# Performance work log

Measured on AMD Instinct MI355X. Metric: run time of the kernel, lower is better.

Reference implementation:

```python
import jax, jax.numpy as jnp
import numpy as np
from jax import lax

DIM = 256
HEADS = 8
DIM_HEAD = 64
INNER = HEADS * DIM_HEAD  # 512
K = 3
PAD = K // 2
KV_STRIDE = 2
SCALE = DIM_HEAD ** -0.5
BN_EPS = 1e-5


def _dw_block(x, w_dw, g, b, m, v, w_pw, stride):
    """depthwise conv -> batchnorm (eval) -> 1x1 conv. x: [B,C,H,W]."""
    c = x.shape[1]
    h = lax.conv_general_dilated(
        x, w_dw, window_strides=(stride, stride),
        padding=[(PAD, PAD), (PAD, PAD)],
        feature_group_count=c,
        dimension_numbers=('NCHW', 'OIHW', 'NCHW'))
    inv = lax.rsqrt(v + BN_EPS)
    h = (h - m[None, :, None, None]) * (g * inv)[None, :, None, None] + b[None, :, None, None]
    return jnp.einsum('oc,bchw->bohw', w_pw, h)


def _heads_flat(t):
    # [B, h*d, H, W] -> [B, h, d, H*W]
    B, hd, H, W = t.shape
    return t.reshape(B, HEADS, DIM_HEAD, H * W)


def _cross_attn(q, k, v, Hq, Wq):
    # q: [B,h,d,i], k/v: [B,h,d,j]
    dots = jnp.einsum('bhdi,bhdj->bhij', q, k) * SCALE
    attn = jax.nn.softmax(dots, axis=-1)
    out = jnp.einsum('bhij,bhdj->bhdi', attn, v)
    B = q.shape[0]
    return out.reshape(B, INNER, Hq, Wq)


def _forward(x, y, q_dw_w, q_bn_gamma, q_bn_beta, q_bn_mean, q_bn_var, q_pw_w,
             kv_dw_w, kv_bn_gamma, kv_bn_beta, kv_bn_mean, kv_bn_var, kv_pw_w,
             out_w, out_b):
    B, _, Hx, Wx = x.shape
    _, _, Hy, Wy = y.shape

    qx = _heads_flat(_dw_block(x, q_dw_w, q_bn_gamma, q_bn_beta, q_bn_mean, q_bn_var, q_pw_w, 1))
    kvx = _dw_block(x, kv_dw_w, kv_bn_gamma, kv_bn_beta, kv_bn_mean, kv_bn_var, kv_pw_w, KV_STRIDE)
    kx, vx = map(_heads_flat, jnp.split(kvx, 2, axis=1))

    qy = _heads_flat(_dw_block(y, q_dw_w, q_bn_gamma, q_bn_beta, q_bn_mean, q_bn_var, q_pw_w, 1))
    kvy = _dw_block(y, kv_dw_w, kv_bn_gamma, kv_bn_beta, kv_bn_mean, kv_bn_var, kv_pw_w, KV_STRIDE)
    ky, vy = map(_heads_flat, jnp.split(kvy, 2, axis=1))

    outx = _cross_attn(qx, ky, vy, Hx, Wx)   # x queries attend to y keys/values
    outy = _cross_attn(qy, kx, vx, Hy, Wy)   # y queries attend to x keys/values

    def proj(o):
        return jnp.einsum('oc,bchw->bohw', out_w, o) + out_b[None, :, None, None]

    return proj(outx), proj(outy)


def setup_inputs() -> dict:
    key = jax.random.key(0)
    ks = jax.random.split(key, 8)
    B, H, W = 8, 32, 32
    return {
        'x': jax.random.normal(ks[0], (B, DIM, H, W), jnp.float32),
        'y': jax.random.normal(ks[1], (B, DIM, H, W), jnp.float32),
        'q_dw_w': jax.random.normal(ks[2], (DIM, 1, K, K), jnp.float32) * 0.1,
        'q_bn_gamma': jnp.ones((DIM,), jnp.float32),
        'q_bn_beta': jnp.zeros((DIM,), jnp.float32),
        'q_bn_mean': jnp.zeros((DIM,), jnp.float32),
        'q_bn_var': jnp.ones((DIM,), jnp.float32),
        'q_pw_w': jax.random.normal(ks[3], (INNER, DIM), jnp.float32) * (DIM ** -0.5),
        'kv_dw_w': jax.random.normal(ks[4], (DIM, 1, K, K), jnp.float32) * 0.1,
        'kv_bn_gamma': jnp.ones((DIM,), jnp.float32),
        'kv_bn_beta': jnp.zeros((DIM,), jnp.float32),
        'kv_bn_mean': jnp.zeros((DIM,), jnp.float32),
        'kv_bn_var': jnp.ones((DIM,), jnp.float32),
        'kv_pw_w': jax.random.normal(ks[5], (2 * INNER, DIM), jnp.float32) * (DIM ** -0.5),
        'out_w': jax.random.normal(ks[6], (DIM, INNER), jnp.float32) * (INNER ** -0.5),
        'out_b': jnp.zeros((DIM,), jnp.float32),
    }


def reference(x, y, q_dw_w, q_bn_gamma, q_bn_beta, q_bn_mean, q_bn_var, q_pw_w,
              kv_dw_w, kv_bn_gamma, kv_bn_beta, kv_bn_mean, kv_bn_var, kv_pw_w,
              out_w, out_b):
    return _forward(x, y, q_dw_w, q_bn_gamma, q_bn_beta, q_bn_mean, q_bn_var, q_pw_w,
                    kv_dw_w, kv_bn_gamma, kv_bn_beta, kv_bn_mean, kv_bn_var, kv_pw_w,
                    out_w, out_b)
```

## Files before the change

### kernel.cpp

```cpp
#include <hip/hip_runtime.h>

#define BN_EPS 1e-5f
#define ATT_SCALE 0.125f

typedef _Float16 half_t;
typedef _Float16 half8 __attribute__((ext_vector_type(8)));
typedef _Float16 half4 __attribute__((ext_vector_type(4)));
typedef float f32x4 __attribute__((ext_vector_type(4)));

__device__ __forceinline__ void gll16(const void* g, void* l) {
    __builtin_amdgcn_global_load_lds((const __attribute__((address_space(1))) void*)g,
                                     (__attribute__((address_space(3))) void*)l, 16, 0, 0);
}

template<int N>
__device__ __forceinline__ void vmwait() {
    asm volatile("s_waitcnt vmcnt(%0)" :: "i"(N) : "memory");
}

__device__ void prep_body8(
    int base, int c,
    const float* qg, const float* qb, const float* qm, const float* qv, const float* qpw,
    const float* kg, const float* kbt, const float* km, const float* kvv, const float* kvpw,
    const float* outw,
    half_t* wq, half_t* wkv, half_t* wout, float* bq, float* bkv, float* red)
{
    #pragma unroll
    for (int oo = 0; oo < 8; ++oo) {
        int o = base + oo;
        if (o >= 1536) {
            int ro = o - 1536;
            #pragma unroll
            for (int ci = 0; ci < 2; ++ci) {
                int cc = ci * 256 + c;
                float wv = outw[(size_t)ro * 512 + cc];
                half_t hh = (half_t)wv;
                wout[(size_t)ro * 1024 + cc]       = hh;
                wout[(size_t)ro * 1024 + 512 + cc] = (half_t)(wv - (float)hh);
            }
            continue;
        }
        const float *g, *b, *m, *v, *w; half_t* we; float* be;
        if (o < 512) {
            g = qg; b = qb; m = qm; v = qv;
            w = qpw + (size_t)o * 256; we = wq + (size_t)o * 512; be = bq + o;
        } else {
            int ro = o - 512;
            g = kg; b = kbt; m = km; v = kvv;
            w = kvpw + (size_t)ro * 256; we = wkv + (size_t)ro * 512; be = bkv + ro;
        }
        float s  = g[c] * rsqrtf(v[c] + BN_EPS);
        float tt = b[c] - m[c] * s;
        float wv = w[c];
        float wsv = wv * s;
        half_t hh = (half_t)wsv;
        we[c]       = hh;
        we[256 + c] = (half_t)(wsv - (float)hh);
        float partial = wv * tt;
        #pragma unroll
        for (int off = 32; off > 0; off >>= 1)
            partial += __shfl_down(partial, off, 64);
        if ((c & 63) == 0) red[c >> 6] = partial;
        __syncthreads();
        if (c == 0) *be = red[0] + red[1] + red[2] + red[3];
        __syncthreads();
    }
}

__device__ void dw_body(
    int rp, int img, int cc, float* sin,
    const float* x, const float* y,
    const float* qdw, const float* kvdw,
    half_t* qB, half_t* kvB)
{
    const float* in = (img < 8) ? x + (size_t)img * 256 * 1024
                                : y + (size_t)(img - 8) * 256 * 1024;
    int t = threadIdx.x;
    int ch = t & 63, cg = t >> 6;
    int r0 = 2 * rp - 1;
    #pragma unroll
    for (int u = t; u < 1024; u += 256) {
        int c = u >> 4, row = (u >> 2) & 3, pi = u & 3;
        sin[c * 148 + row * 36 + (pi < 2 ? pi : 32 + pi)] = 0.f;
    }
    #pragma unroll
    for (int ii = 0; ii < 8; ++ii) {
        int u = ii * 256 + t;
        int sch = u >> 5, row = (u >> 3) & 3, seg = u & 7;
        int gr = r0 + row;
        float4 v4 = {0.f, 0.f, 0.f, 0.f};
        if (gr >= 0 && gr < 32)
            v4 = *(const float4*)(in + (size_t)(cc * 64 + sch) * 1024 + gr * 32 + seg * 4);
        float* d = &sin[sch * 148 + row * 36 + 2 + seg * 4];
        d[0] = v4.x; d[1] = v4.y; d[2] = v4.z; d[3] = v4.w;
    }
    __syncthreads();
    int gch = cc * 64 + ch;
    float wq9[9], wk9[9];
    #pragma unroll
    for (int i = 0; i < 9; ++i) { wq9[i] = qdw[gch * 9 + i]; wk9[i] = kvdw[gch * 9 + i]; }
    float rowv[4][12];
    const float* base = &sin[ch * 148];
    #pragma unroll
    for (int rr = 0; rr < 4; ++rr) {
        *(float4*)&rowv[rr][0] = *(const float4*)(base + rr * 36 + cg * 8);
        *(float4*)&rowv[rr][4] = *(const float4*)(base + rr * 36 + cg * 8 + 4);
        *(float4*)&rowv[rr][8] = *(const float4*)(base + rr * 36 + cg * 8 + 8);
    }
    #pragma unroll
    for (int r = 0; r < 2; ++r) {
        #pragma unroll
        for (int c8 = 0; c8 < 8; ++c8) {
            float acc = 0.f;
            #pragma unroll
            for (int dr = 0; dr < 3; ++dr)
                #pragma unroll
                for (int dc = 0; dc < 3; ++dc)
                    acc += wq9[dr * 3 + dc] * rowv[r + dr][c8 + dc + 1];
            half_t hh = (half_t)acc;
            size_t p = (size_t)img * 1024 + (2 * rp + r) * 32 + cg * 8 + c8;
            qB[p * 512 + gch]       = hh;
            qB[p * 512 + 256 + gch] = (half_t)(acc - (float)hh);
        }
    }
    #pragma unroll
    for (int c4 = 0; c4 < 4; ++c4) {
        float acc = 0.f;
        #pragma unroll
        for (int dr = 0; dr < 3; ++dr)
            #pragma unroll
            for (int dc = 0; dc < 3; ++dc)
                acc += wk9[dr * 3 + dc] * rowv[dr][2 * c4 + dc + 1];
        half_t hh = (half_t)acc;
        size_t p = (size_t)img * 256 + rp * 16 + cg * 4 + c4;
        kvB[p * 512 + gch]       = hh;
        kvB[p * 512 + 256 + gch] = (half_t)(acc - (float)hh);
    }
}

__global__ __launch_bounds__(256) void prep_dw_kernel(
    const float* __restrict__ x, const float* __restrict__ y,
    const float* __restrict__ qdw, const float* __restrict__ kvdw,
    const float* __restrict__ qg, const float* __restrict__ qb,
    const float* __restrict__ qm, const float* __restrict__ qv,
    const float* __restrict__ qpw,
    const float* __restrict__ kg, const float* __restrict__ kbt,
    const float* __restrict__ km, const float* __restrict__ kvv,
    const float* __restrict__ kvpw,
    const float* __restrict__ outw,
    half_t* __restrict__ wq, half_t* __restrict__ wkv, half_t* __restrict__ wout,
    float* __restrict__ bq, float* __restrict__ bkv,
    half_t* __restrict__ qB, half_t* __restrict__ kvB)
{
    __shared__ __align__(16) float smem[64 * 148];
    int bx = blockIdx.x;
    if (bx < 1024)
        dw_body((bx >> 4) & 15, bx & 15, bx >> 8, smem, x, y, qdw, kvdw, qB, kvB);
    else
        prep_body8((bx - 1024) * 8, threadIdx.x, qg, qb, qm, qv, qpw,
                   kg, kbt, km, kvv, kvpw, outw, wq, wkv, wout, bq, bkv, smem);
}

template<int MT, int NT, int WGM, int WGN, int NTHR, int MODE, int KTOT>
__device__ __forceinline__ void gemm_worker(
    char* lds, const half_t* Ab, const half_t* Bb,
    void* outBuf, const float* bias,
    int NPX, int img, int m0, int n0, float scale)
{
    constexpr int TM = WGM * MT * 16, TN = WGN * NT * 16;
    constexpr int BUF = (TM + TN) * 128;
    constexpr int NC = KTOT / 32;
    constexpr int GCNT = 8 * (TM + TN) / NTHR;
    int t = threadIdx.x, w = t >> 6, lane = t & 63, quad = lane >> 4, l15 = lane & 15;
    int wm = w % WGM, wn = w / WGM;
    f32x4 acc[MT][NT] = {};

    auto stage = [&](int kh, int p) {
        char* Ah = lds + p * BUF;
        char* Al = Ah + TM * 64;
        char* Bh = Ah + TM * 128;
        char* Bl = Bh + TN * 64;
        #pragma unroll
        for (int ii = 0; ii < TM * 4 / NTHR; ++ii) {
            int u = ii * NTHR + t;
            int mt = u >> 6, q = (u >> 4) & 3, r = u & 15;
            const half_t* g = Ab + (size_t)(mt * 16 + r) * (2 * KTOT) + kh + q * 8;
            gll16(g,        Ah + (u & ~63) * 16);
            gll16(g + KTOT, Al + (u & ~63) * 16);
        }
        #pragma unroll
        for (int ii = 0; ii < TN * 4 / NTHR; ++ii) {
            int u = ii * NTHR + t;
            int nt = u >> 6, q = (u >> 4) & 3, r = u & 15;
            const half_t* g = Bb + (size_t)(nt * 16 + r) * (2 * KTOT) + kh + q * 8;
            gll16(g,        Bh + (u & ~63) * 16);
            gll16(g + KTOT, Bl + (u & ~63) * 16);
        }
    };

    stage(0, 0);
    for (int kc = 0; kc < NC; ++kc) {
        if (kc + 1 < NC) { stage((kc + 1) * 32, (kc + 1) & 1); vmwait<GCNT>(); }
        else             { vmwait<0>(); }
        __builtin_amdgcn_s_barrier();
        __builtin_amdgcn_sched_barrier(0);
        char* Ah = lds + (kc & 1) * BUF;
        char* Al = Ah + TM * 64;
        char* Bh = Ah + TM * 128;
        char* Bl = Bh + TN * 64;
        half8 afh[MT], afl[MT];
        #pragma unroll
        for (int mi = 0; mi < MT; ++mi) {
            afh[mi] = *(half8*)(Ah + (wm * MT + mi) * 1024 + lane * 16);
            afl[mi] = *(half8*)(Al + (wm * MT + mi) * 1024 + lane * 16);
        }
        __builtin_amdgcn_s_setprio(1);
        #pragma unroll
        for (int ni = 0; ni < NT; ++ni) {
            half8 bh = *(half8*)(Bh + (wn * NT + ni) * 1024 + lane * 16);
            half8 bl = *(half8*)(Bl + (wn * NT + ni) * 1024 + lane * 16);
            #pragma unroll
            for (int mi = 0; mi < MT; ++mi) {
                acc[mi][ni] = __builtin_amdgcn_mfma_f32_16x16x32_f16(afh[mi], bh, acc[mi][ni], 0, 0, 0);
                acc[mi][ni] = __builtin_amdgcn_mfma_f32_16x16x32_f16(afh[mi], bl, acc[mi][ni], 0, 0, 0);
                acc[mi][ni] = __builtin_amdgcn_mfma_f32_16x16x32_f16(afl[mi], bh, acc[mi][ni], 0, 0, 0);
            }
        }
        __builtin_amdgcn_s_setprio(0);
        __builtin_amdgcn_s_barrier();
        __builtin_amdgcn_sched_barrier(0);
    }

    if (MODE == 2) {
        #pragma unroll
        for (int mi = 0; mi < MT; ++mi) {
            int mrow0 = m0 + wm * MT * 16 + mi * 16 + quad * 4;
            #pragma unroll
            for (int ni = 0; ni < NT; ++ni) {
                int col = n0 + wn * NT * 16 + ni * 16 + l15;
                f32x4 a = acc[mi][ni];
                float* op = (float*)outBuf + (size_t)img * 256 * NPX;
                #pragma unroll
                for (int r = 0; r < 4; ++r)
                    op[(size_t)(mrow0 + r) * NPX + col] = a[r] + bias[mrow0 + r];
            }
        }
    } else {
        __syncthreads();
        float* tbuf = (float*)lds;
        constexpr int TP = 40;
        #pragma unroll
        for (int qtr = 0; qtr < TM / 32; ++qtr) {
            #pragma unroll
            for (int mi = 0; mi < MT; ++mi) {
                int rowblk = wm * MT * 16 + mi * 16;
                if (rowblk >= qtr * 32 && rowblk < qtr * 32 + 32) {
                    int mloc = rowblk - qtr * 32 + quad * 4;
                    #pragma unroll
                    for (int ni = 0; ni < NT; ++ni) {
                        int nloc = wn * NT * 16 + ni * 16 + l15;
                        #pragma unroll
                        for (int r = 0; r < 4; ++r) {
                            float vv = acc[mi][ni][r];
                            if (MODE == 0) vv = (vv + bias[m0 + rowblk + quad * 4 + r]) * scale;
                            else           vv = vv + bias[n0 + nloc];
                            tbuf[nloc * TP + mloc + r] = vv;
                        }
                    }
                }
            }
            __syncthreads();
            #pragma unroll
            for (int it = 0; it < (TN * 4) / NTHR; ++it) {
                int u = it * NTHR + t;
                int n = u >> 2, mg = u & 3;
                float vv[8];
                *(float4*)&vv[0] = *(const float4*)&tbuf[n * TP + mg * 8];
                *(float4*)&vv[4] = *(const float4*)&tbuf[n * TP + mg * 8 + 4];
                half8 hv, lv;
                #pragma unroll
                for (int j = 0; j < 8; ++j) {
                    half_t hh = (half_t)vv[j];
                    hv[j] = hh; lv[j] = (half_t)(vv[j] - (float)hh);
                }
                int mglob = m0 + qtr * 32 + mg * 8;
                if (MODE == 0) {
                    int h = mglob >> 6, d0 = mglob & 63;
                    half_t* op = (half_t*)outBuf + ((size_t)(img * 8 + h) * NPX + n0 + n) * 128 + d0;
                    *(half8*)op = hv;
                    *(half8*)(op + 64) = lv;
                } else {
                    int nn = n0 + n, h = nn >> 6, d = nn & 63;
                    int j0 = mglob;
                    half_t* op = (half_t*)outBuf + (size_t)(img * 8 + h) * 32768
                               + (j0 >> 5) * 4096 + ((d >> 4) & 3) * 512 + ((j0 >> 4) & 1) * 256
                               + ((j0 >> 2) & 3) * 64 + (d & 15) * 4;
                    half4 a0 = {hv[0], hv[1], hv[2], hv[3]};
                    half4 a1 = {hv[4], hv[5], hv[6], hv[7]};
                    half4 b0 = {lv[0], lv[1], lv[2], lv[3]};
                    half4 b1 = {lv[4], lv[5], lv[6], lv[7]};
                    *(half4*)op               = a0;
                    *(half4*)(op + 64)        = a1;
                    *(half4*)(op + 2048)      = b0;
                    *(half4*)(op + 2048 + 64) = b1;
                }
            }
            __syncthreads();
        }
    }
}

__global__ __launch_bounds__(512, 4) void qkv_kernel(
    const half_t* __restrict__ wq, const half_t* __restrict__ wkv,
    const half_t* __restrict__ qB, const half_t* __restrict__ kvB,
    const float* __restrict__ bq, const float* __restrict__ bkv,
    half_t* __restrict__ qpr, half_t* __restrict__ kpr, half_t* __restrict__ vpr)
{
    __shared__ __align__(16) char lds[65536];
    int tile = blockIdx.x, img = blockIdx.z;
    if (tile < 32) {
        int m0 = (tile >> 3) * 128, n0 = (tile & 7) * 128;
        gemm_worker<2, 4, 4, 2, 512, 0, 256>(lds,
            wq + (size_t)m0 * 512,
            qB + (size_t)img * (1024 * 512) + (size_t)n0 * 512,
            qpr, bq, 1024, img, m0, n0, ATT_SCALE);
    } else if (tile < 40) {
        int tt = tile - 32;
        int m0 = (tt >> 1) * 128, n0 = (tt & 1) * 128;
        gemm_worker<2, 4, 4, 2, 512, 0, 256>(lds,
            wkv + (size_t)m0 * 512,
            kvB + (size_t)img * (256 * 512) + (size_t)n0 * 512,
            kpr, bkv, 256, img, m0, n0, 1.0f);
    } else {
        int tt = tile - 40;
        int m0 = (tt >> 2) * 128, n0 = (tt & 3) * 128;
        gemm_worker<2, 4, 4, 2, 512, 1, 256>(lds,
            kvB + (size_t)img * (256 * 512) + (size_t)m0 * 512,
            wkv + (size_t)(512 + n0) * 512,
            vpr, bkv + 512, 512, img, m0, n0, 1.0f);
    }
}

__global__ __launch_bounds__(512, 4) void out_kernel(
    const half_t* __restrict__ wout, const half_t* __restrict__ attp,
    const float* __restrict__ outb, float* __restrict__ out)
{
    __shared__ __align__(16) char lds[65536];
    int tile = blockIdx.x, img = blockIdx.z;
    int m0 = (tile >> 3) * 128, n0 = (tile & 7) * 128;
    gemm_worker<2, 4, 4, 2, 512, 2, 512>(lds,
        wout + (size_t)m0 * 1024,
        attp + (size_t)img * (1024 * 1024) + (size_t)n0 * 1024,
        out, outb, 1024, img, m0, n0, 1.0f);
}

__global__ __launch_bounds__(512, 4) void attn_fused(
    const half_t* __restrict__ qb, const half_t* __restrict__ kb,
    const half_t* __restrict__ vb, half_t* __restrict__ att)
{
    __shared__ __align__(16) char lds[33792];
    int ic = blockIdx.y;
    int img = blockIdx.x & 15, h = blockIdx.x >> 4;
    int partner = img ^ 8;
    int t = threadIdx.x, w = t >> 6, lane = t & 63, quad = lane >> 4, l15 = lane & 15;
    const half_t* qp = qb + ((size_t)(img * 8 + h) * 1024 + ic * 128) * 128;
    const half_t* kp = kb + (size_t)(partner * 8 + h) * 256 * 128;
    const half_t* vp = vb + (size_t)(partner * 8 + h) * 32768;

    half8 qh[2], ql[2];
    #pragma unroll
    for (int kcs = 0; kcs < 2; ++kcs) {
        const half_t* qr = qp + (size_t)(w * 16 + l15) * 128 + kcs * 32 + quad * 8;
        qh[kcs] = *(const half8*)qr;
        ql[kcs] = *(const half8*)(qr + 64);
    }

    auto stageC = [&](int c) {
        char* buf = lds + (c & 3) * 8192;
        if (c < 8) {
            int sb = t >> 6, li = t & 63;
            int plane = sb >> 2, ntr = (sb >> 1) & 1, kcs = sb & 1;
            const half_t* g = kp + (size_t)(c * 32 + ntr * 16 + (li & 15)) * 128
                                 + plane * 64 + kcs * 32 + (li >> 4) * 8;
            gll16(g, buf + (t & ~63) * 16);
        } else {
            gll16(vp + (size_t)(c - 8) * 4096 + t * 8, buf + (t & ~63) * 16);
        }
    };

    f32x4 sacc[16] = {};
    f32x4 oacc[4] = {};
    float mx = 0.f, lsum = 0.f;

    stageC(0); stageC(1); stageC(2);

    #pragma unroll
    for (int c = 0; c < 16; ++c) {
        if (c < 14)       vmwait<2>();
        else if (c == 14) vmwait<1>();
        else              vmwait<0>();
        __builtin_amdgcn_s_barrier();
        __builtin_amdgcn_sched_barrier(0);
        if (c + 3 < 16) stageC(c + 3);
        const char* buf = lds + (c & 3) * 8192;
        if (c < 8) {
            __builtin_amdgcn_s_setprio(1);
            #pragma unroll
            for (int kcs = 0; kcs < 2; ++kcs)
                #pragma unroll
                for (int ntr = 0; ntr < 2; ++ntr) {
                    half8 kh = *(const half8*)(buf + (ntr * 2 + kcs) * 1024 + lane * 16);
                    half8 kl = *(const half8*)(buf + 4096 + (ntr * 2 + kcs) * 1024 + lane * 16);
                    f32x4 s = sacc[c * 2 + ntr];
                    s = __builtin_amdgcn_mfma_f32_16x16x32_f16(kh, qh[kcs], s, 0, 0, 0);
                    s = __builtin_amdgcn_mfma_f32_16x16x32_f16(kh, ql[kcs], s, 0, 0, 0);
                    s = __builtin_amdgcn_mfma_f32_16x16x32_f16(kl, qh[kcs], s, 0, 0, 0);
                    sacc[c * 2 + ntr] = s;
                }
            __builtin_amdgcn_s_setprio(0);
        } else {
            if (c == 8) {
                float m_ = sacc[0][0];
                #pragma unroll
                for (int ti = 0; ti < 16; ++ti)
                    #pragma unroll
                    for (int r = 0; r < 4; ++r) m_ = fmaxf(m_, sacc[ti][r]);
                m_ = fmaxf(m_, __shfl_xor(m_, 16, 64));
                mx = fmaxf(m_, __shfl_xor(m_, 32, 64));
            }
            int jc = c - 8;
            half4 pb[2][2];
            #pragma unroll
            for (int kk = 0; kk < 2; ++kk) {
                f32x4 s = sacc[jc * 2 + kk];
                #pragma unroll
                for (int e = 0; e < 4; ++e) {
                    float pv = __expf(s[e] - mx);
                    lsum += pv;
                    half_t hh = (half_t)pv;
                    pb[kk][0][e] = hh;
                    pb[kk][1][e] = (half_t)(pv - (float)hh);
                }
            }
            __builtin_amdgcn_s_setprio(1);
            #pragma unroll
            for (int mt = 0; mt < 4; ++mt) {
                #pragma unroll
                for (int kk = 0; kk < 2; ++kk) {
                    half4 vh = *(const half4*)(buf + (mt * 2 + kk) * 512 + lane * 8);
                    half4 vl = *(const half4*)(buf + 4096 + (mt * 2 + kk) * 512 + lane * 8);
                    f32x4 o = oacc[mt];
                    o = __builtin_amdgcn_mfma_f32_16x16x16f16(vh, pb[kk][0], o, 0, 0, 0);
                    o = __builtin_amdgcn_mfma_f32_16x16x16f16(vh, pb[kk][1], o, 0, 0, 0);
                    o = __builtin_amdgcn_mfma_f32_16x16x16f16(vl, pb[kk][0], o, 0, 0, 0);
                    oacc[mt] = o;
                }
            }
            __builtin_amdgcn_s_setprio(0);
        }
    }

    lsum += __shfl_xor(lsum, 16, 64);
    lsum += __shfl_xor(lsum, 32, 64);
    float inv = 1.f / lsum;

    __syncthreads();
    #pragma unroll
    for (int mt = 0; mt < 4; ++mt)
        #pragma unroll
        for (int r = 0; r < 4; ++r) {
            float vv = oacc[mt][r] * inv;
            half_t hh = (half_t)vv;
            int row = w * 16 + l15;
            int d = mt * 16 + quad * 4 + r;
            *(half_t*)(lds + (row * 132 + d) * 2)      = hh;
            *(half_t*)(lds + (row * 132 + 64 + d) * 2) = (half_t)(vv - (float)hh);
        }
    __syncthreads();
    #pragma unroll
    for (int ii = 0; ii < 4; ++ii) {
        int u = ii * 512 + t;
        int i = u >> 4, seg = (u >> 3) & 1, p8 = u & 7;
        half8 val = *(const half8*)(lds + (i * 132 + seg * 64 + p8 * 8) * 2);
        *(half8*)(att + ((size_t)img * 1024 + ic * 128 + i) * 1024
                  + seg * 512 + h * 64 + p8 * 8) = val;
    }
}

extern "C" void kernel_launch(void* const* d_in, const int* in_sizes, int n_in,
                              void* d_out, int out_size, void* d_ws, size_t ws_size,
                              hipStream_t stream) {
    const float* x    = (const float*)d_in[0];
    const float* y    = (const float*)d_in[1];
    const float* qdw  = (const float*)d_in[2];
    const float* qg   = (const float*)d_in[3];
    const float* qbb  = (const float*)d_in[4];
    const float* qm   = (const float*)d_in[5];
    const float* qv   = (const float*)d_in[6];
    const float* qpw  = (const float*)d_in[7];
    const float* kvdw = (const float*)d_in[8];
    const float* kg   = (const float*)d_in[9];
    const float* kb_  = (const float*)d_in[10];
    const float* km   = (const float*)d_in[11];
    const float* kvv  = (const float*)d_in[12];
    const float* kvpw = (const float*)d_in[13];
    const float* outw = (const float*)d_in[14];
    const float* outb = (const float*)d_in[15];

    char* ws = (char*)d_ws;
    half_t* wq   = (half_t*)(ws);
    half_t* wkv  = (half_t*)(ws + 524288);
    half_t* wout = (half_t*)(ws + 1572864);
    float*  bq   = (float*) (ws + 2097152);
    float*  bkv  = (float*) (ws + 2099200);
    half_t* qpr  = (half_t*)(ws + 2103296);
    half_t* kpr  = (half_t*)(ws + 35657728);
    half_t* vpr  = (half_t*)(ws + 44046336);
    half_t* qB   = (half_t*)(ws + 52434944);
    half_t* kvB  = (half_t*)(ws + 69212160);
    half_t* attp = (half_t*)(ws + 52434944);

    prep_dw_kernel<<<1248, 256, 0, stream>>>(
        x, y, qdw, kvdw, qg, qbb, qm, qv, qpw, kg, kb_, km, kvv, kvpw, outw,
        wq, wkv, wout, bq, bkv, qB, kvB);

    qkv_kernel<<<dim3(48, 1, 16), 512, 0, stream>>>(
        wq, wkv, qB, kvB, bq, bkv, qpr, kpr, vpr);

    attn_fused<<<dim3(128, 8, 1), 512, 0, stream>>>(qpr, kpr, vpr, attp);

    out_kernel<<<dim3(16, 1, 16), 512, 0, stream>>>(wout, attp, outb, (float*)d_out);
}
```

Measured before the change: 197.7 us.

## Replace out-projection GEMM with dedicated 128x64 tile kernel and doubled grid

The output projection no longer goes through the generic gemm_worker. It now has its own kernel with 128x64 tiles, a double-buffered LDS pipeline filled by direct global-to-LDS loads, and 2x2 MFMA tiles per warp, launched on twice as many blocks. The MODE 2 epilogue in gemm_worker is removed because nothing uses it anymore. The aim is more blocks to spread across CUs and better latency hiding, at the cost of less data reuse per tile and more reloading of the weight tiles.

```diff
diff --git a/kernel.cpp b/kernel.cpp
--- a/kernel.cpp
+++ b/kernel.cpp
@@ -231,82 +231,66 @@
         __builtin_amdgcn_sched_barrier(0);
     }
 
-    if (MODE == 2) {
+    __syncthreads();
+    float* tbuf = (float*)lds;
+    constexpr int TP = 40;
+    #pragma unroll
+    for (int qtr = 0; qtr < TM / 32; ++qtr) {
         #pragma unroll
         for (int mi = 0; mi < MT; ++mi) {
-            int mrow0 = m0 + wm * MT * 16 + mi * 16 + quad * 4;
-            #pragma unroll
-            for (int ni = 0; ni < NT; ++ni) {
-                int col = n0 + wn * NT * 16 + ni * 16 + l15;
-                f32x4 a = acc[mi][ni];
-                float* op = (float*)outBuf + (size_t)img * 256 * NPX;
+            int rowblk = wm * MT * 16 + mi * 16;
+            if (rowblk >= qtr * 32 && rowblk < qtr * 32 + 32) {
+                int mloc = rowblk - qtr * 32 + quad * 4;
                 #pragma unroll
-                for (int r = 0; r < 4; ++r)
-                    op[(size_t)(mrow0 + r) * NPX + col] = a[r] + bias[mrow0 + r];
-            }
-        }
-    } else {
-        __syncthreads();
-        float* tbuf = (float*)lds;
-        constexpr int TP = 40;
-        #pragma unroll
-        for (int qtr = 0; qtr < TM / 32; ++qtr) {
-            #pragma unroll
-            for (int mi = 0; mi < MT; ++mi) {
-                int rowblk = wm * MT * 16 + mi * 16;
-                if (rowblk >= qtr * 32 && rowblk < qtr * 32 + 32) {
-                    int mloc = rowblk - qtr * 32 + quad * 4;
+                for (int ni = 0; ni < NT; ++ni) {
+                    int nloc = wn * NT * 16 + ni * 16 + l15;
                     #pragma unroll
-                    for (int ni = 0; ni < NT; ++ni) {
-                        int nloc = wn * NT * 16 + ni * 16 + l15;
-                        #pragma unroll
-                        for (int r = 0; r < 4; ++r) {
-                            float vv = acc[mi][ni][r];
-                            if (MODE == 0) vv = (vv + bias[m0 + rowblk + quad * 4 + r]) * scale;
-                            else           vv = vv + bias[n0 + nloc];
-                            tbuf[nloc * TP + mloc + r] = vv;
-                        }
+                    for (int r = 0; r < 4; ++r) {
+                        float vv = acc[mi][ni][r];
+                        if (MODE == 0) vv = (vv + bias[m0 + rowblk + quad * 4 + r]) * scale;
+                        else           vv = vv + bias[n0 + nloc];
+                        tbuf[nloc * TP + mloc + r] = vv;
                     }
                 }
             }
-            __syncthreads();
-            #pragma unroll
-            for (int it = 0; it < (TN * 4) / NTHR; ++it) {
-                int u = it * NTHR + t;
-                int n = u >> 2, mg = u & 3;
-                float vv[8];
-                *(float4*)&vv[0] = *(const float4*)&tbuf[n * TP + mg * 8];
-                *(float4*)&vv[4] = *(const float4*)&tbuf[n * TP + mg * 8 + 4];
-                half8 hv, lv;
-                #pragma unroll
-                for (int j = 0; j < 8; ++j) {
-                    half_t hh = (half_t)vv[j];
-                    hv[j] = hh; lv[j] = (half_t)(vv[j] - (float)hh);
-                }
-                int mglob = m0 + qtr * 32 + mg * 8;
-                if (MODE == 0) {
-                    int h = mglob >> 6, d0 = mglob & 63;
-                    half_t* op = (half_t*)outBuf + ((size_t)(img * 8 + h) * NPX + n0 + n) * 128 + d0;
-                    *(half8*)op = hv;
-                    *(half8*)(op + 64) = lv;
-                } else {
-                    int nn = n0 + n, h = nn >> 6, d = nn & 63;
-                    int j0 = mglob;
-                    half_t* op = (half_t*)outBuf + (size_t)(img * 8 + h) * 32768
-                               + (j0 >> 5) * 4096 + ((d >> 4) & 3) * 512 + ((j0 >> 4) & 1) * 256
-                               + ((j0 >> 2) & 3) * 64 + (d & 15) * 4;
-                    half4 a0 = {hv[0], hv[1], hv[2], hv[3]};
-                    half4 a1 = {hv[4], hv[5], hv[6], hv[7]};
-                    half4 b0 = {lv[0], lv[1], lv[2], lv[3]};
-                    half4 b1 = {lv[4], lv[5], lv[6], lv[7]};
-                    *(half4*)op               = a0;
-                    *(half4*)(op + 64)        = a1;
-                    *(half4*)(op + 2048)      = b0;
-                    *(half4*)(op + 2048 + 64) = b1;
-                }
-            }
-            __syncthreads();
-        }
+        }
+        __syncthreads();
+        #pragma unroll
+        for (int it = 0; it < (TN * 4) / NTHR; ++it) {
+            int u = it * NTHR + t;
+            int n = u >> 2, mg = u & 3;
+            float vv[8];
+            *(float4*)&vv[0] = *(const float4*)&tbuf[n * TP + mg * 8];
+            *(float4*)&vv[4] = *(const float4*)&tbuf[n * TP + mg * 8 + 4];
+            half8 hv, lv;
+            #pragma unroll
+            for (int j = 0; j < 8; ++j) {
+                half_t hh = (half_t)vv[j];
+                hv[j] = hh; lv[j] = (half_t)(vv[j] - (float)hh);
+            }
+            int mglob = m0 + qtr * 32 + mg * 8;
+            if (MODE == 0) {
+                int h = mglob >> 6, d0 = mglob & 63;
+                half_t* op = (half_t*)outBuf + ((size_t)(img * 8 + h) * NPX + n0 + n) * 128 + d0;
+                *(half8*)op = hv;
+                *(half8*)(op + 64) = lv;
+            } else {
+                int nn = n0 + n, h = nn >> 6, d = nn & 63;
+                int j0 = mglob;
+                half_t* op = (half_t*)outBuf + (size_t)(img * 8 + h) * 32768
+                           + (j0 >> 5) * 4096 + ((d >> 4) & 3) * 512 + ((j0 >> 4) & 1) * 256
+                           + ((j0 >> 2) & 3) * 64 + (d & 15) * 4;
+                half4 a0 = {hv[0], hv[1], hv[2], hv[3]};
+                half4 a1 = {hv[4], hv[5], hv[6], hv[7]};
+                half4 b0 = {lv[0], lv[1], lv[2], lv[3]};
+                half4 b1 = {lv[4], lv[5], lv[6], lv[7]};
+                *(half4*)op               = a0;
+                *(half4*)(op + 64)        = a1;
+                *(half4*)(op + 2048)      = b0;
+                *(half4*)(op + 2048 + 64) = b1;
+            }
+        }
+        __syncthreads();
     }
 }
 
@@ -345,13 +329,86 @@
     const half_t* __restrict__ wout, const half_t* __restrict__ attp,
     const float* __restrict__ outb, float* __restrict__ out)
 {
-    __shared__ __align__(16) char lds[65536];
+    __shared__ __align__(16) char lds[49152];
+    constexpr int KTOT = 512, NC = 16, BUF = 24576;
     int tile = blockIdx.x, img = blockIdx.z;
-    int m0 = (tile >> 3) * 128, n0 = (tile & 7) * 128;
-    gemm_worker<2, 4, 4, 2, 512, 2, 512>(lds,
-        wout + (size_t)m0 * 1024,
-        attp + (size_t)img * (1024 * 1024) + (size_t)n0 * 1024,
-        out, outb, 1024, img, m0, n0, 1.0f);
+    int m0 = (tile >> 4) * 128, n0 = (tile & 15) * 64;
+    const half_t* Ab = wout + (size_t)m0 * 1024;
+    const half_t* Bb = attp + (size_t)img * (1024 * 1024) + (size_t)n0 * 1024;
+
+    int t = threadIdx.x, w = t >> 6, lane = t & 63, quad = lane >> 4, l15 = lane & 15;
+    int wm = w & 3, wn = w >> 2;
+    f32x4 acc[2][2] = {};
+
+    auto stage = [&](int kh, int p) {
+        char* Ah = lds + p * BUF;
+        char* Al = Ah + 8192;
+        char* Bh = Ah + 16384;
+        char* Bl = Ah + 20480;
+        {
+            int mt = t >> 6, q = (t >> 4) & 3, r = t & 15;
+            const half_t* g = Ab + (size_t)(mt * 16 + r) * (2 * KTOT) + kh + q * 8;
+            gll16(g,        Ah + (t & ~63) * 16);
+            gll16(g + KTOT, Al + (t & ~63) * 16);
+        }
+        if (t < 256) {
+            int nt = t >> 6, q = (t >> 4) & 3, r = t & 15;
+            const half_t* g = Bb + (size_t)(nt * 16 + r) * (2 * KTOT) + kh + q * 8;
+            gll16(g,        Bh + (t & ~63) * 16);
+            gll16(g + KTOT, Bl + (t & ~63) * 16);
+        }
+    };
+
+    stage(0, 0);
+    for (int kc = 0; kc < NC; ++kc) {
+        if (kc + 1 < NC) {
+            stage((kc + 1) * 32, (kc + 1) & 1);
+            if (t < 256) vmwait<4>(); else vmwait<2>();
+        } else {
+            vmwait<0>();
+        }
+        __builtin_amdgcn_s_barrier();
+        __builtin_amdgcn_sched_barrier(0);
+        char* Ah = lds + (kc & 1) * BUF;
+        char* Al = Ah + 8192;
+        char* Bh = Ah + 16384;
+        char* Bl = Ah + 20480;
+        half8 afh[2], afl[2];
+        #pragma unroll
+        for (int mi = 0; mi < 2; ++mi) {
+            afh[mi] = *(half8*)(Ah + (wm * 2 + mi) * 1024 + lane * 16);
+            afl[mi] = *(half8*)(Al + (wm * 2 + mi) * 1024 + lane * 16);
+        }
+        __builtin_amdgcn_s_setprio(1);
+        #pragma unroll
+        for (int ni = 0; ni < 2; ++ni) {
+            half8 bh = *(half8*)(Bh + (wn * 2 + ni) * 1024 + lane * 16);
+            half8 bl = *(half8*)(Bl + (wn * 2 + ni) * 1024 + lane * 16);
+            #pragma unroll
+            for (int mi = 0; mi < 2; ++mi) {
+                acc[mi][ni] = __builtin_amdgcn_mfma_f32_16x16x32_f16(afh[mi], bh, acc[mi][ni], 0, 0, 0);
+                acc[mi][ni] = __builtin_amdgcn_mfma_f32_16x16x32_f16(afh[mi], bl, acc[mi][ni], 0, 0, 0);
+                acc[mi][ni] = __builtin_amdgcn_mfma_f32_16x16x32_f16(afl[mi], bh, acc[mi][ni], 0, 0, 0);
+            }
+        }
+        __builtin_amdgcn_s_setprio(0);
+        __builtin_amdgcn_s_barrier();
+        __builtin_amdgcn_sched_barrier(0);
+    }
+
+    float* op = out + (size_t)img * 256 * 1024;
+    #pragma unroll
+    for (int mi = 0; mi < 2; ++mi) {
+        int mrow0 = m0 + (wm * 2 + mi) * 16 + quad * 4;
+        #pragma unroll
+        for (int ni = 0; ni < 2; ++ni) {
+            int col = n0 + (wn * 2 + ni) * 16 + l15;
+            f32x4 a = acc[mi][ni];
+            #pragma unroll
+            for (int r = 0; r < 4; ++r)
+                op[(size_t)(mrow0 + r) * 1024 + col] = a[r] + outb[mrow0 + r];
+        }
+    }
 }
 
 __global__ __launch_bounds__(512, 4) void attn_fused(
@@ -529,5 +586,5 @@
 
     attn_fused<<<dim3(128, 8, 1), 512, 0, stream>>>(qpr, kpr, vpr, attp);
 
-    out_kernel<<<dim3(16, 1, 16), 512, 0, stream>>>(wout, attp, outb, (float*)d_out);
-}
+    out_kernel<<<dim3(32, 1, 16), 512, 0, stream>>>(wout, attp, outb, (float*)d_out);
+}
```

Result: slower. 202.5 us (+2.5%).
